# Performance work log

Measured on AMD Instinct MI355X. Metric: run time of the kernel, lower is better.

The kernel has to match this reference:

```python
import jax, jax.numpy as jnp
import numpy as np

B, N, C, L = 2, 128, 256, 3
NODE_IN, EDGE_IN = 128, 64
KN, KE = 101, 7
ALPHA = 0.2
EPS = 1e-5

def lrelu(x):
    return jax.nn.leaky_relu(x, ALPHA)

def layer_norm(x, g, b):
    mu = jnp.mean(x, axis=-1, keepdims=True)
    var = jnp.mean((x - mu) ** 2, axis=-1, keepdims=True)
    return (x - mu) / jnp.sqrt(var + EPS) * g + b

def setup_inputs() -> dict:
    key = jax.random.key(0)
    ks = jax.random.split(key, 20)
    s = 0.05
    nodes = jax.random.normal(ks[0], (B, N, NODE_IN), jnp.float32)
    edges = jax.random.normal(ks[1], (B, N, N, EDGE_IN), jnp.float32)
    m = (jax.random.uniform(ks[2], (B, N, N)) > 0.3).astype(jnp.float32)
    adj_mask = jnp.maximum(m, jnp.eye(N, dtype=jnp.float32)[None])  # guarantee non-empty rows
    return {
        'nodes': nodes, 'edges': edges, 'adj_mask': adj_mask,
        'pnW': jax.random.normal(ks[3], (C, NODE_IN)) * s, 'pnb': jnp.zeros((C,)),
        'peW': jax.random.normal(ks[4], (C, EDGE_IN)) * s, 'peb': jnp.zeros((C,)),
        'Wb': jax.random.normal(ks[5], (L, C, 3 * C)) * s,
        'Wbp': jax.random.normal(ks[6], (L, C, C)) * s,
        'Wfp': jax.random.normal(ks[7], (L, C, C)) * s,
        'ub': jax.random.normal(ks[8], (L, C)) * s,
        'Wf': jax.random.normal(ks[9], (L, C, C)) * s,
        'eln_g': jnp.ones((L, C)), 'eln_b': jnp.zeros((L, C)),
        'nln_g': jnp.ones((L, C)), 'nln_b': jnp.zeros((L, C)),
        'ncW': jax.random.normal(ks[10], (KN, C)) * s, 'ncb': jnp.zeros((KN,)),
        'ecW': jax.random.normal(ks[11], (KE, C)) * s, 'ecb': jnp.zeros((KE,)),
    }

def reference(nodes, edges, adj_mask, pnW, pnb, peW, peb, Wb, Wbp, Wfp, ub, Wf,
              eln_g, eln_b, nln_g, nln_b, ncW, ncb, ecW, ecb):
    nodes = nodes @ pnW.T + pnb          # (B,N,C)
    edges = edges @ peW.T + peb          # (B,N,N,C)
    mask3 = adj_mask[..., None]
    for l in range(Wb.shape[0]):
        Cd = nodes.shape[-1]
        Wb1, Wb2, Wb3 = Wb[l][:, :Cd], Wb[l][:, Cd:2 * Cd], Wb[l][:, 2 * Cd:]
        # W_b([f_i, edges, f_j]) without materializing the (B,N,N,3C) concat
        ai = nodes @ Wb1.T                # (B,N,C) broadcast along j
        aj = nodes @ Wb3.T                # (B,N,C) broadcast along i
        ne = lrelu(ai[:, :, None, :] + edges @ Wb2.T + aj[:, None, :, :])
        ne = ne * mask3
        new_edges = layer_norm(ne + edges, eln_g[l], eln_b[l])
        edges_in = jnp.swapaxes(new_edges, 1, 2)      # permute(0,2,1,3)
        tn = nodes @ Wfp[l].T             # shared by term_node_i / term_node_j
        st = edges_in @ Wbp[l].T + tn[:, :, None, :] + tn[:, None, :, :]
        r = lrelu(st @ ub[l])             # (B,N,N)
        r = jnp.where(adj_mask > 0, r, -jnp.inf)
        attn = jnp.nan_to_num(jax.nn.softmax(r, axis=2))
        agg = jnp.einsum('bij,bjd->bid', attn, nodes @ Wf[l].T)
        nodes = layer_norm(lrelu(agg) + nodes, nln_g[l], nln_b[l])
        edges = new_edges
    node_logits = nodes @ ncW.T + ncb
    edge_logits = edges @ ecW.T + ecb
    return (nodes, edges, node_logits, edge_logits)
```

## Files before the change

kernel.cpp:

```cpp
#include <hip/hip_runtime.h>
#include <hip/hip_bf16.h>


#define ALPHA 0.2f
#define EPS_ 1e-5f

typedef __hip_bfloat16 bf16;
typedef __bf16 bf16x8 __attribute__((ext_vector_type(8)));
typedef __bf16 bf16x4 __attribute__((ext_vector_type(4)));
typedef float floatx4 __attribute__((ext_vector_type(4)));

__device__ __forceinline__ float bf2f(bf16 x){ return __bfloat162float(x); }
__device__ __forceinline__ bf16  f2bf(float x){ return __float2bfloat16(x); }
__device__ __forceinline__ float lrelu_f(float x){ return x > 0.f ? x : ALPHA * x; }

#define T_NODES 0u
#define T_EDGES 32768u
#define T_ADJ   2129920u
#define T_PNW   2162688u
#define T_PNB   2195456u
#define T_PEW   2195712u
#define T_PEB   2212096u
#define T_WB    2212352u
#define T_WBP   2802176u
#define T_WFP   2998784u
#define T_UB    3195392u
#define T_WF    3196160u
#define T_ELNG  3392768u
#define T_ELNB  3393536u
#define T_NLNG  3394304u
#define T_NLNB  3395072u
#define T_NCW   3395840u
#define T_NCB   3421696u
#define T_ECW   3421800u
#define T_ECB   3423592u

#define O_NODES 0u
#define O_EDGES 65536u
#define O_NLOG  8454144u
#define O_ELOG  8480000u

struct SrcPtrs { const void* p[20]; };

__device__ __forceinline__ float rawld(const void* p, size_t i, bool isb){
    return isb ? bf2f(((const bf16*)p)[i]) : ((const float*)p)[i];
}

__device__ __forceinline__ bf16x8 ldfrag8(const void* p, size_t e, bool isb){
    if (isb) return *reinterpret_cast<const bf16x8*>((const bf16*)p + e);
    const float4* f = (const float4*)((const float*)p + e);
    float4 a = f[0], b = f[1];
    bf16 o[8];
    o[0]=f2bf(a.x); o[1]=f2bf(a.y); o[2]=f2bf(a.z); o[3]=f2bf(a.w);
    o[4]=f2bf(b.x); o[5]=f2bf(b.y); o[6]=f2bf(b.z); o[7]=f2bf(b.w);
    return *reinterpret_cast<bf16x8*>(o);
}

__global__ __launch_bounds__(256) void setup_k(SrcPtrs sp, bf16* __restrict__ canon,
                                               float* __restrict__ vbuf, float* __restrict__ wbuf,
                                               float* __restrict__ nodes_cur,
                                               bf16* __restrict__ rw2, bf16* __restrict__ rpe){
    const unsigned short* probe = (const unsigned short*)sp.p[12];
    const bool isb = (probe[0] == 0x3F80);
    int blk = blockIdx.x, tid = threadIdx.x;
    int wave = tid >> 6, lane = tid & 63, quad = lane >> 4, l16 = lane & 15;

    if (blk < 1024){
        const unsigned COFF[20] = {T_NODES,T_EDGES,T_ADJ,T_PNW,T_PNB,T_PEW,T_PEB,T_WB,T_WBP,T_WFP,
                                   T_UB,T_WF,T_ELNG,T_ELNB,T_NLNG,T_NLNB,T_NCW,T_NCB,T_ECW,T_ECB};
        const unsigned SZ[20]   = {32768u,2097152u,32768u,32768u,256u,16384u,256u,589824u,196608u,196608u,
                                   768u,196608u,768u,768u,768u,768u,25856u,101u,1792u,7u};
        unsigned gtid = blk*256u + tid;
        unsigned gstride = 1024u*256u;
        for (int t = 0; t < 20; ++t){
            const void* src = sp.p[t];
            unsigned coff = COFF[t], n = SZ[t];
            unsigned chunks = n >> 3;
            if (isb){
                const uint4* s4 = (const uint4*)src;
                for (unsigned idx = gtid; idx < chunks; idx += gstride)
                    *reinterpret_cast<uint4*>(canon + coff + idx*8u) = s4[idx];
            } else {
                const float4* s4 = (const float4*)src;
                for (unsigned idx = gtid; idx < chunks; idx += gstride){
                    float4 a = s4[2*idx], b = s4[2*idx+1];
                    bf16 o[8];
                    o[0]=f2bf(a.x); o[1]=f2bf(a.y); o[2]=f2bf(a.z); o[3]=f2bf(a.w);
                    o[4]=f2bf(b.x); o[5]=f2bf(b.y); o[6]=f2bf(b.z); o[7]=f2bf(b.w);
                    *reinterpret_cast<uint4*>(canon + coff + idx*8u) = *reinterpret_cast<uint4*>(o);
                }
            }
            unsigned tail = n & 7u;
            if (gtid < tail){
                unsigned li = chunks*8u + gtid;
                canon[coff + li] = isb ? ((const bf16*)src)[li] : f2bf(((const float*)src)[li]);
            }
        }
    } else if (blk < 1030){
        int q = blk - 1024;
        int l = q >> 1, m = q & 1;
        const void* W = m ? sp.p[9] : sp.p[8];
        float* out = (m ? wbuf : vbuf) + l*256;
        int c = tid;
        __shared__ float shu[256];
        shu[c] = rawld(sp.p[10], l*256 + c, isb);
        __syncthreads();
        float a0=0.f, a1=0.f, a2=0.f, a3=0.f;
        for (int cp0 = 0; cp0 < 256; cp0 += 16){
#pragma unroll
            for (int j = 0; j < 16; ++j){
                float wv = rawld(W, (size_t)l*65536u + (size_t)(cp0+j)*256u + c, isb);
                float pr = shu[cp0+j] * wv;
                if ((j & 3) == 0) a0 += pr;
                else if ((j & 3) == 1) a1 += pr;
                else if ((j & 3) == 2) a2 += pr;
                else a3 += pr;
            }
        }
        out[c] = (a0 + a1) + (a2 + a3);
    } else if (blk < 1038){
        int row0 = (blk - 1030) * 32;
        floatx4 acc[2][4] = {};
#pragma unroll
        for (int k0c = 0; k0c < 4; ++k0c){
            int k0 = k0c*32;
            bf16x8 a[2], bb[4];
#pragma unroll
            for (int mt = 0; mt < 2; ++mt)
                a[mt] = ldfrag8(sp.p[0], (size_t)(row0 + mt*16 + l16)*128u + k0 + quad*8, isb);
#pragma unroll
            for (int nt = 0; nt < 4; ++nt)
                bb[nt] = ldfrag8(sp.p[3], (size_t)(wave*64 + nt*16 + l16)*128u + k0 + quad*8, isb);
#pragma unroll
            for (int mt = 0; mt < 2; ++mt)
#pragma unroll
                for (int nt = 0; nt < 4; ++nt)
                    acc[mt][nt] = __builtin_amdgcn_mfma_f32_16x16x32_bf16(a[mt], bb[nt], acc[mt][nt], 0, 0, 0);
        }
#pragma unroll
        for (int nt = 0; nt < 4; ++nt){
            int n = wave*64 + nt*16 + l16;
            float bn = rawld(sp.p[4], n, isb);
#pragma unroll
            for (int mt = 0; mt < 2; ++mt)
#pragma unroll
                for (int reg = 0; reg < 4; ++reg){
                    int r = row0 + mt*16 + quad*4 + reg;
                    nodes_cur[r*256 + n] = acc[mt][nt][reg] + bn;
                }
        }
    } else if (blk < 1086){
        int rb = blk - 1038;
        int l = rb >> 4, n_tile = rb & 15;
        bf16* dst = rw2 + l*65536;
#pragma unroll
        for (int half = 0; half < 2; ++half){
            int slot = half*256 + tid;
            int k0c = slot >> 6, ln = slot & 63;
            int qd = ln >> 4, lw = ln & 15;
            int n = n_tile*16 + lw;
            bf16 o[8];
#pragma unroll
            for (int j = 0; j < 8; ++j){
                int k = k0c*32 + qd*8 + j;
                o[j] = f2bf(rawld(sp.p[7], (size_t)l*196608u + (size_t)n*768u + 256u + k, isb));
            }
            *reinterpret_cast<uint4*>(dst + ((k0c*16 + n_tile)*64 + ln)*8) = *reinterpret_cast<uint4*>(o);
        }
    } else {
        int n_tile = blk - 1086;
        if (tid < 128){
            int slot = tid;
            int k0c = slot >> 6, ln = slot & 63;
            int qd = ln >> 4, lw = ln & 15;
            int n = n_tile*16 + lw;
            bf16 o[8];
#pragma unroll
            for (int j = 0; j < 8; ++j){
                int k = k0c*32 + qd*8 + j;
                o[j] = f2bf(rawld(sp.p[5], (size_t)n*64u + k, isb));
            }
            *reinterpret_cast<uint4*>(rpe + ((n_tile*2 + k0c)*64 + ln)*8) = *reinterpret_cast<uint4*>(o);
        }
    }
}

__global__ __launch_bounds__(256) void node_linears_k(
        const float* __restrict__ nodes_cur, const bf16* __restrict__ Wb_l,
        const bf16* __restrict__ Wf_l, const float* __restrict__ w_l,
        float* __restrict__ ai, float* __restrict__ aj,
        float* __restrict__ nf, float* __restrict__ s){
    int row = blockIdx.x;
    int c = threadIdx.x;
    __shared__ float x[256];
    __shared__ float red[4];
    x[c] = nodes_cur[row*256 + c];
    __syncthreads();
    float xs = x[c] * w_l[c];
    for (int off = 32; off; off >>= 1) xs += __shfl_xor(xs, off, 64);
    if ((c & 63) == 0) red[c >> 6] = xs;
    const bf16x8* w1 = reinterpret_cast<const bf16x8*>(Wb_l + (size_t)c*768);
    const bf16x8* w3 = reinterpret_cast<const bf16x8*>(Wb_l + (size_t)c*768 + 512);
    const bf16x8* wf = reinterpret_cast<const bf16x8*>(Wf_l + (size_t)c*256);
    float a1 = 0.f, a3 = 0.f, f = 0.f;
#pragma unroll 4
    for (int ch = 0; ch < 32; ++ch){
        bf16x8 v1 = w1[ch], v3 = w3[ch], vf = wf[ch];
#pragma unroll
        for (int j = 0; j < 8; ++j){
            float xv = x[ch*8 + j];
            a1 += xv * (float)v1[j];
            a3 += xv * (float)v3[j];
            f  += xv * (float)vf[j];
        }
    }
    ai[row*256 + c] = a1;
    aj[row*256 + c] = a3;
    nf[row*256 + c] = f;
    __syncthreads();
    if (c == 0) s[row] = red[0] + red[1] + red[2] + red[3];
}

__global__ __launch_bounds__(256) void edge_update2_k(
        bf16* __restrict__ Ebuf, const bf16* __restrict__ rw2_l,
        const float* __restrict__ ai, const float* __restrict__ aj,
        const bf16* __restrict__ adj, const bf16* __restrict__ g, const bf16* __restrict__ bta,
        const float* __restrict__ v, float* __restrict__ rbuf,
        int isfinal, const bf16* __restrict__ ecW, const bf16* __restrict__ ecb,
        void* __restrict__ dout, const unsigned short* __restrict__ probe,
        int isfirst, const bf16* __restrict__ eIn, const bf16* __restrict__ rpe,
        const bf16* __restrict__ peb){
    int row0 = blockIdx.x * 64;
    int b = row0 >> 14, i = (row0 >> 7) & 127, j0 = row0 & 127;
    int tid = threadIdx.x;
    int wave = tid >> 6, lane = tid & 63, quad = lane >> 4, l16 = lane & 15;

    __shared__ bf16  shA[64*264];
    __shared__ float sh_ai[256];
    __shared__ float sh_v[256];
    __shared__ float sh_g[256];
    __shared__ float sh_bt[256];
    __shared__ float sh_w7[7][256];
    __shared__ float smS[4][64];
    __shared__ float smQ[4][64];
    __shared__ float dvp[4][64];
    __shared__ float lgp[4][64][7];

    sh_ai[tid] = ai[(b*128 + i)*256 + tid];
    sh_v[tid]  = v[tid];
    sh_g[tid]  = bf2f(g[tid]);
    sh_bt[tid] = bf2f(bta[tid]);
    if (isfirst){
        floatx4 pacc[4][4] = {};
#pragma unroll
        for (int k0c = 0; k0c < 2; ++k0c){
            int k0 = k0c*32;
            bf16x8 a[4], bb[4];
#pragma unroll
            for (int mt = 0; mt < 4; ++mt)
                a[mt] = *reinterpret_cast<const bf16x8*>(eIn + (size_t)(row0 + mt*16 + l16)*64 + k0 + quad*8);
#pragma unroll
            for (int nt = 0; nt < 4; ++nt)
                bb[nt] = *reinterpret_cast<const bf16x8*>(rpe + ((size_t)((wave*4 + nt)*2 + k0c)*64 + lane)*8);
#pragma unroll
            for (int mt = 0; mt < 4; ++mt)
#pragma unroll
                for (int nt = 0; nt < 4; ++nt)
                    pacc[mt][nt] = __builtin_amdgcn_mfma_f32_16x16x32_bf16(a[mt], bb[nt], pacc[mt][nt], 0, 0, 0);
        }
#pragma unroll
        for (int nt = 0; nt < 4; ++nt){
            int col = wave*64 + nt*16 + l16;
            float bbv = bf2f(peb[col]);
#pragma unroll
            for (int mt = 0; mt < 4; ++mt)
#pragma unroll
                for (int reg = 0; reg < 4; ++reg)
                    shA[(mt*16 + quad*4 + reg)*264 + col] = f2bf(pacc[mt][nt][reg] + bbv);
        }
    } else {
#pragma unroll
        for (int it = 0; it < 8; ++it){
            int idx = it*256 + tid;
            int r = idx >> 5, c8 = idx & 31;
            bf16x8 vA = *reinterpret_cast<const bf16x8*>(Ebuf + (size_t)(row0 + r)*256 + c8*8);
            *reinterpret_cast<bf16x8*>(&shA[r*264 + c8*8]) = vA;
        }
    }
    if (isfinal){
        for (int idx = tid; idx < 7*256; idx += 256)
            sh_w7[idx >> 8][idx & 255] = bf2f(ecW[idx]);
    }
    __syncthreads();

    floatx4 acc[4][4] = {};
    {
        const bf16* shb = &shA[l16*264];
        for (int k0c = 0; k0c < 8; ++k0c){
            bf16x8 bfr[4];
#pragma unroll
            for (int rf = 0; rf < 4; ++rf)
                bfr[rf] = *reinterpret_cast<const bf16x8*>(shb + rf*16*264 + k0c*32 + quad*8);
#pragma unroll
            for (int mt = 0; mt < 4; ++mt){
                bf16x8 afrag = *reinterpret_cast<const bf16x8*>(
                    rw2_l + ((size_t)(k0c*16 + wave*4 + mt)*64 + lane)*8);
#pragma unroll
                for (int rf = 0; rf < 4; ++rf)
                    acc[mt][rf] = __builtin_amdgcn_mfma_f32_16x16x32_bf16(afrag, bfr[rf], acc[mt][rf], 0, 0, 0);
            }
        }
    }

    const bool isb = (probe[0] == 0x3F80);
    float maskv[4];
#pragma unroll
    for (int rf = 0; rf < 4; ++rf){
        int rl = rf*16 + l16;
        int j  = j0 + rl;
        maskv[rf] = bf2f(adj[(b*128 + i)*128 + j]);
        const float* ajrow = aj + (size_t)(b*128 + j)*256;
        float s = 0.f, q = 0.f;
#pragma unroll
        for (int mt = 0; mt < 4; ++mt){
            int c0 = wave*64 + mt*16 + quad*4;
            float4 ajv = *reinterpret_cast<const float4*>(ajrow + c0);
            float4 aiv = *reinterpret_cast<const float4*>(sh_ai + c0);
            bf16x4 ev  = *reinterpret_cast<const bf16x4*>(&shA[rl*264 + c0]);
#pragma unroll
            for (int reg = 0; reg < 4; ++reg){
                float y = acc[mt][rf][reg] + ((const float*)&aiv)[reg] + ((const float*)&ajv)[reg];
                float x = lrelu_f(y) * maskv[rf] + (float)ev[reg];
                acc[mt][rf][reg] = x;
                s += x; q += x*x;
            }
        }
        s += __shfl_xor(s, 16, 64); s += __shfl_xor(s, 32, 64);
        q += __shfl_xor(q, 16, 64); q += __shfl_xor(q, 32, 64);
        if (quad == 0){ smS[wave][rl] = s; smQ[wave][rl] = q; }
    }
    __syncthreads();

#pragma unroll
    for (int rf = 0; rf < 4; ++rf){
        int rl = rf*16 + l16;
        int j  = j0 + rl;
        int grow = row0 + rl;
        float ts = smS[0][rl] + smS[1][rl] + smS[2][rl] + smS[3][rl];
        float tq = smQ[0][rl] + smQ[1][rl] + smQ[2][rl] + smQ[3][rl];
        float mu  = ts * (1.f/256.f);
        float var = tq * (1.f/256.f) - mu*mu;
        float rstd = rsqrtf(var + EPS_);
        float dv = 0.f;
        float lg[7] = {0.f,0.f,0.f,0.f,0.f,0.f,0.f};
#pragma unroll
        for (int mt = 0; mt < 4; ++mt){
            int c0 = wave*64 + mt*16 + quad*4;
            float4 gv = *reinterpret_cast<const float4*>(sh_g + c0);
            float4 bv = *reinterpret_cast<const float4*>(sh_bt + c0);
            float4 vv = *reinterpret_cast<const float4*>(sh_v + c0);
            float xo4[4];
#pragma unroll
            for (int reg = 0; reg < 4; ++reg){
                float xo = (acc[mt][rf][reg] - mu) * rstd * ((const float*)&gv)[reg] + ((const float*)&bv)[reg];
                xo4[reg] = xo;
                dv += xo * ((const float*)&vv)[reg];
            }
            if (!isfinal){
                bf16x4 ob;
#pragma unroll
                for (int reg = 0; reg < 4; ++reg) ob[reg] = f2bf(xo4[reg]);
                *reinterpret_cast<bf16x4*>(Ebuf + (size_t)grow*256 + c0) = ob;
            } else {
                if (isb){
                    bf16x4 ob;
#pragma unroll
                    for (int reg = 0; reg < 4; ++reg) ob[reg] = f2bf(xo4[reg]);
                    *reinterpret_cast<bf16x4*>((bf16*)dout + O_EDGES + (size_t)grow*256 + c0) = ob;
                } else {
                    float4 of;
                    of.x = xo4[0]; of.y = xo4[1]; of.z = xo4[2]; of.w = xo4[3];
                    *reinterpret_cast<float4*>((float*)dout + O_EDGES + (size_t)grow*256 + c0) = of;
                }
#pragma unroll
                for (int k = 0; k < 7; ++k){
                    const float* w7r = &sh_w7[k][c0];
#pragma unroll
                    for (int reg = 0; reg < 4; ++reg) lg[k] += xo4[reg] * w7r[reg];
                }
            }
        }
        dv += __shfl_xor(dv, 16, 64); dv += __shfl_xor(dv, 32, 64);
        if (quad == 0) dvp[wave][rl] = dv;
        if (isfinal){
#pragma unroll
            for (int k = 0; k < 7; ++k){
                lg[k] += __shfl_xor(lg[k], 16, 64);
                lg[k] += __shfl_xor(lg[k], 32, 64);
            }
            if (quad == 0){
#pragma unroll
                for (int k = 0; k < 7; ++k) lgp[wave][rl][k] = lg[k];
            }
        }
    }
    __syncthreads();

    if (wave == 0 && quad == 0){
#pragma unroll
        for (int rf = 0; rf < 4; ++rf){
            int rl = rf*16 + l16;
            int j  = j0 + rl;
            int grow = row0 + rl;
            float d = dvp[0][rl] + dvp[1][rl] + dvp[2][rl] + dvp[3][rl];
            rbuf[(b*128 + j)*128 + i] = d;
            if (isfinal){
#pragma unroll
                for (int k = 0; k < 7; ++k){
                    float val = lgp[0][rl][k] + lgp[1][rl][k] + lgp[2][rl][k] + lgp[3][rl][k] + bf2f(ecb[k]);
                    if (isb) ((bf16*)dout)[O_ELOG + (size_t)grow*7 + k] = f2bf(val);
                    else     ((float*)dout)[O_ELOG + (size_t)grow*7 + k] = val;
                }
            }
        }
    }
}

__global__ __launch_bounds__(256) void node_update_k(
        const float* __restrict__ rbuf, const float* __restrict__ s_in, const bf16* __restrict__ adj,
        const float* __restrict__ nf_in, float* __restrict__ nodes_cur,
        const bf16* __restrict__ g, const bf16* __restrict__ bta,
        int isfinal,
        const bf16* __restrict__ Wb_nx, const bf16* __restrict__ Wf_nx, const float* __restrict__ w_nx,
        float* __restrict__ ai_o, float* __restrict__ aj_o, float* __restrict__ nf_o, float* __restrict__ s_o,
        const bf16* __restrict__ ncW, const bf16* __restrict__ ncb,
        void* __restrict__ dout, const unsigned short* __restrict__ probe){
    int row = blockIdx.x;
    int b = row >> 7;
    int tid = threadIdx.x;
    int wave = tid >> 6, lane = tid & 63;
    __shared__ float attn[128];
    __shared__ float shr[16];
    __shared__ float shfx[256];

    float rv = -__builtin_inff();
    if (tid < 128){
        float t = rbuf[row*128 + tid] + s_in[row] + s_in[b*128 + tid];
        t = lrelu_f(t);
        rv = (bf2f(adj[row*128 + tid]) > 0.f) ? t : -__builtin_inff();
    }
    float m = rv;
    for (int off = 32; off; off >>= 1) m = fmaxf(m, __shfl_xor(m, off, 64));
    if (lane == 0) shr[wave] = m;
    __syncthreads();
    float mx = fmaxf(fmaxf(shr[0], shr[1]), fmaxf(shr[2], shr[3]));
    float e = (tid < 128 && rv > -__builtin_inff()) ? expf(rv - mx) : 0.f;
    if (tid < 128) attn[tid] = e;
    float se = e;
    for (int off = 32; off; off >>= 1) se += __shfl_xor(se, off, 64);
    if (lane == 0) shr[4 + wave] = se;
    __syncthreads();
    float inv = 1.f / (shr[4] + shr[5] + shr[6] + shr[7]);

    int c = tid;
    const float* nfb = nf_in + (size_t)b*32768 + c;
    float g0 = 0.f, g1 = 0.f, g2 = 0.f, g3 = 0.f;
    float g4 = 0.f, g5 = 0.f, g6 = 0.f, g7 = 0.f;
    for (int jj = 0; jj < 128; jj += 8){
        g0 += attn[jj]   * nfb[(size_t)jj*256];
        g1 += attn[jj+1] * nfb[(size_t)(jj+1)*256];
        g2 += attn[jj+2] * nfb[(size_t)(jj+2)*256];
        g3 += attn[jj+3] * nfb[(size_t)(jj+3)*256];
        g4 += attn[jj+4] * nfb[(size_t)(jj+4)*256];
        g5 += attn[jj+5] * nfb[(size_t)(jj+5)*256];
        g6 += attn[jj+6] * nfb[(size_t)(jj+6)*256];
        g7 += attn[jj+7] * nfb[(size_t)(jj+7)*256];
    }
    float agg = (((g0 + g1) + (g2 + g3)) + ((g4 + g5) + (g6 + g7))) * inv;
    float x = lrelu_f(agg) + nodes_cur[row*256 + c];
    float xs = x, xq = x*x;
    for (int off = 32; off; off >>= 1){ xs += __shfl_xor(xs, off, 64); xq += __shfl_xor(xq, off, 64); }
    if (lane == 0){ shr[8 + wave] = xs; shr[12 + wave] = xq; }
    __syncthreads();
    float sum = shr[8] + shr[9] + shr[10] + shr[11];
    float sq  = shr[12] + shr[13] + shr[14] + shr[15];
    float mu  = sum * (1.f/256.f);
    float var = sq * (1.f/256.f) - mu*mu;
    float rstd = rsqrtf(var + EPS_);
    float out = (x - mu) * rstd * bf2f(g[c]) + bf2f(bta[c]);
    nodes_cur[row*256 + c] = out;
    shfx[c] = out;
    __syncthreads();

    if (!isfinal){
        float ws2 = out * w_nx[c];
        for (int off = 32; off; off >>= 1) ws2 += __shfl_xor(ws2, off, 64);
        if (lane == 0) shr[wave] = ws2;
        const bf16x8* w1 = reinterpret_cast<const bf16x8*>(Wb_nx + (size_t)c*768);
        const bf16x8* w3 = reinterpret_cast<const bf16x8*>(Wb_nx + (size_t)c*768 + 512);
        const bf16x8* wf = reinterpret_cast<const bf16x8*>(Wf_nx + (size_t)c*256);
        float a1 = 0.f, a3 = 0.f, f = 0.f;
#pragma unroll 4
        for (int ch = 0; ch < 32; ++ch){
            bf16x8 v1 = w1[ch], v3 = w3[ch], vf = wf[ch];
#pragma unroll
            for (int j = 0; j < 8; ++j){
                float xv = shfx[ch*8 + j];
                a1 += xv * (float)v1[j];
                a3 += xv * (float)v3[j];
                f  += xv * (float)vf[j];
            }
        }
        ai_o[row*256 + c] = a1;
        aj_o[row*256 + c] = a3;
        nf_o[row*256 + c] = f;
        __syncthreads();
        if (c == 0) s_o[row] = shr[0] + shr[1] + shr[2] + shr[3];
    } else {
        const bool isb = (probe[0] == 0x3F80);
        if (isb) ((bf16*)dout)[O_NODES + row*256 + c] = f2bf(out);
        else     ((float*)dout)[O_NODES + row*256 + c] = out;
        if (tid < 101){
            const bf16x8* wr = reinterpret_cast<const bf16x8*>(ncW + (size_t)tid*256);
            float acc = bf2f(ncb[tid]);
#pragma unroll 4
            for (int ch = 0; ch < 32; ++ch){
                bf16x8 wv = wr[ch];
#pragma unroll
                for (int j = 0; j < 8; ++j) acc += shfx[ch*8 + j] * (float)wv[j];
            }
            if (isb) ((bf16*)dout)[O_NLOG + row*101 + tid] = f2bf(acc);
            else     ((float*)dout)[O_NLOG + row*101 + tid] = acc;
        }
    }
}

extern "C" void kernel_launch(void* const* d_in, const int* in_sizes, int n_in,
                              void* d_out, int out_size, void* d_ws, size_t ws_size,
                              hipStream_t stream){
    (void)in_sizes; (void)n_in; (void)out_size; (void)ws_size;

    SrcPtrs sp;
    for (int i = 0; i < 20; ++i) sp.p[i] = d_in[i];
    const unsigned short* probe = (const unsigned short*)d_in[12];

    bf16* canon = (bf16*)d_ws;
    char* ws2 = (char*)d_ws + 6847488;
    bf16* Ebuf = (bf16*)ws2;
    float* f = (float*)(ws2 + 16777216);
    float* ai    = f;
    float* aj    = f + 65536;
    float* nfA   = f + 131072;
    float* nfB   = f + 196608;
    float* sA    = f + 262144;
    float* sB    = f + 262400;
    float* rbuf  = f + 262656;
    float* vbuf  = f + 295424;
    float* wbuf  = f + 296192;
    float* nodes_cur = f + 296960;
    bf16* rw2 = (bf16*)(f + 362496);
    bf16* rpe = rw2 + 196608;

    const bf16* c_edges = canon + T_EDGES;
    const bf16* c_adj   = canon + T_ADJ;
    const bf16* c_peb   = canon + T_PEB;
    const bf16* c_Wb    = canon + T_WB;
    const bf16* c_Wf    = canon + T_WF;
    const bf16* c_elng  = canon + T_ELNG;
    const bf16* c_elnb  = canon + T_ELNB;
    const bf16* c_nlng  = canon + T_NLNG;
    const bf16* c_nlnb  = canon + T_NLNB;
    const bf16* c_ncW   = canon + T_NCW;
    const bf16* c_ncb   = canon + T_NCB;
    const bf16* c_ecW   = canon + T_ECW;
    const bf16* c_ecb   = canon + T_ECB;

    setup_k<<<dim3(1102), dim3(256), 0, stream>>>(sp, canon, vbuf, wbuf, nodes_cur, rw2, rpe);
    node_linears_k<<<dim3(256), dim3(256), 0, stream>>>(
        nodes_cur, c_Wb, c_Wf, wbuf, ai, aj, nfA, sA);

    for (int l = 0; l < 3; ++l){
        int fin = (l == 2);
        int fst = (l == 0);
        float* nf_in = (l & 1) ? nfB : nfA;
        float* nf_out = (l & 1) ? nfA : nfB;
        float* s_in  = (l & 1) ? sB : sA;
        float* s_out = (l & 1) ? sA : sB;
        edge_update2_k<<<dim3(512), dim3(256), 0, stream>>>(
            Ebuf, rw2 + l*65536, ai, aj, c_adj,
            c_elng + l*256, c_elnb + l*256, vbuf + l*256, rbuf,
            fin, c_ecW, c_ecb, d_out, probe,
            fst, c_edges, rpe, c_peb);
        node_update_k <<<dim3(256), dim3(256), 0, stream>>>(
            rbuf, s_in, c_adj, nf_in, nodes_cur, c_nlng + l*256, c_nlnb + l*256,
            fin,
            c_Wb + (size_t)(l+1)*196608, c_Wf + (size_t)(l+1)*65536, wbuf + (l+1)*256,
            ai, aj, nf_out, s_out,
            c_ncW, c_ncb, d_out, probe);
    }
}
```

Measured before the change: 274.5 us.

## Move node linears to MFMA kernel and halve edge tile rows

The per-row scalar node linear projections (ai, aj, nf) are replaced by a separate MFMA-based kernel that processes 32 rows per block, and they are no longer fused into node_update_k. The edge update kernel now handles 32 rows per block instead of 64, with twice the blocks and a launch-bounds occupancy hint, and it prefetches the aj values and mask early. This trades extra kernel launches and lower per-block reuse of the rw2 weights for tensor-core node GEMMs and more parallelism and occupancy in the edge kernel. The linears kernel runs only 8 blocks, which may underuse the GPU, and node inputs are now rounded to bf16 before the product.

Measured after the change: 327.0 us. 19.1% more time.

```diff
diff --git a/kernel.cpp b/kernel.cpp
--- a/kernel.cpp
+++ b/kernel.cpp
@@ -185,43 +185,76 @@
     }
 }
 
-__global__ __launch_bounds__(256) void node_linears_k(
-        const float* __restrict__ nodes_cur, const bf16* __restrict__ Wb_l,
-        const bf16* __restrict__ Wf_l, const float* __restrict__ w_l,
+__global__ __launch_bounds__(256) void linears_k(
+        const float* __restrict__ nodes_cur,
+        const bf16* __restrict__ Wb_l, const bf16* __restrict__ Wf_l,
+        const float* __restrict__ w_l,
         float* __restrict__ ai, float* __restrict__ aj,
         float* __restrict__ nf, float* __restrict__ s){
-    int row = blockIdx.x;
-    int c = threadIdx.x;
-    __shared__ float x[256];
-    __shared__ float red[4];
-    x[c] = nodes_cur[row*256 + c];
+    int row0 = blockIdx.x * 32;
+    int tid = threadIdx.x;
+    int wave = tid >> 6, lane = tid & 63, quad = lane >> 4, l16 = lane & 15;
+    __shared__ bf16 shX[32*264];
+
+#pragma unroll
+    for (int it = 0; it < 4; ++it){
+        int idx = it*256 + tid;
+        int r = idx >> 5, c8 = idx & 31;
+        const float4* fp = (const float4*)(nodes_cur + (size_t)(row0 + r)*256 + c8*8);
+        float4 a = fp[0], b2 = fp[1];
+        bf16 o[8];
+        o[0]=f2bf(a.x); o[1]=f2bf(a.y); o[2]=f2bf(a.z); o[3]=f2bf(a.w);
+        o[4]=f2bf(b2.x); o[5]=f2bf(b2.y); o[6]=f2bf(b2.z); o[7]=f2bf(b2.w);
+        *reinterpret_cast<uint4*>(&shX[r*264 + c8*8]) = *reinterpret_cast<uint4*>(o);
+    }
     __syncthreads();
-    float xs = x[c] * w_l[c];
-    for (int off = 32; off; off >>= 1) xs += __shfl_xor(xs, off, 64);
-    if ((c & 63) == 0) red[c >> 6] = xs;
-    const bf16x8* w1 = reinterpret_cast<const bf16x8*>(Wb_l + (size_t)c*768);
-    const bf16x8* w3 = reinterpret_cast<const bf16x8*>(Wb_l + (size_t)c*768 + 512);
-    const bf16x8* wf = reinterpret_cast<const bf16x8*>(Wf_l + (size_t)c*256);
-    float a1 = 0.f, a3 = 0.f, f = 0.f;
-#pragma unroll 4
-    for (int ch = 0; ch < 32; ++ch){
-        bf16x8 v1 = w1[ch], v3 = w3[ch], vf = wf[ch];
-#pragma unroll
-        for (int j = 0; j < 8; ++j){
-            float xv = x[ch*8 + j];
-            a1 += xv * (float)v1[j];
-            a3 += xv * (float)v3[j];
-            f  += xv * (float)vf[j];
-        }
-    }
-    ai[row*256 + c] = a1;
-    aj[row*256 + c] = a3;
-    nf[row*256 + c] = f;
-    __syncthreads();
-    if (c == 0) s[row] = red[0] + red[1] + red[2] + red[3];
+
+    floatx4 acc[2][12] = {};
+    for (int k0c = 0; k0c < 8; ++k0c){
+        int k0 = k0c*32 + quad*8;
+        bf16x8 a[2];
+#pragma unroll
+        for (int mt = 0; mt < 2; ++mt)
+            a[mt] = *reinterpret_cast<const bf16x8*>(&shX[(mt*16 + l16)*264 + k0]);
+#pragma unroll
+        for (int nt = 0; nt < 12; ++nt){
+            int t = wave*12 + nt;
+            int n = (t & 15)*16 + l16;
+            const bf16* bp;
+            if (t < 16)      bp = Wb_l + (size_t)n*768 + k0;
+            else if (t < 32) bp = Wb_l + (size_t)n*768 + 512 + k0;
+            else             bp = Wf_l + (size_t)n*256 + k0;
+            bf16x8 bb = *reinterpret_cast<const bf16x8*>(bp);
+#pragma unroll
+            for (int mt = 0; mt < 2; ++mt)
+                acc[mt][nt] = __builtin_amdgcn_mfma_f32_16x16x32_bf16(a[mt], bb, acc[mt][nt], 0, 0, 0);
+        }
+    }
+#pragma unroll
+    for (int nt = 0; nt < 12; ++nt){
+        int t = wave*12 + nt;
+        int n = (t & 15)*16 + l16;
+        float* out = (t < 16) ? ai : (t < 32) ? aj : nf;
+#pragma unroll
+        for (int mt = 0; mt < 2; ++mt)
+#pragma unroll
+            for (int reg = 0; reg < 4; ++reg)
+                out[(size_t)(row0 + mt*16 + quad*4 + reg)*256 + n] = acc[mt][nt][reg];
+    }
+    if (tid < 32){
+        const bf16* xr = &shX[tid*264];
+        float a0=0.f, a1=0.f, a2=0.f, a3=0.f;
+        for (int c = 0; c < 256; c += 4){
+            a0 += (float)xr[c]   * w_l[c];
+            a1 += (float)xr[c+1] * w_l[c+1];
+            a2 += (float)xr[c+2] * w_l[c+2];
+            a3 += (float)xr[c+3] * w_l[c+3];
+        }
+        s[row0 + tid] = (a0 + a1) + (a2 + a3);
+    }
 }
 
-__global__ __launch_bounds__(256) void edge_update2_k(
+__global__ __launch_bounds__(256, 3) void edge_update2_k(
         bf16* __restrict__ Ebuf, const bf16* __restrict__ rw2_l,
         const float* __restrict__ ai, const float* __restrict__ aj,
         const bf16* __restrict__ adj, const bf16* __restrict__ g, const bf16* __restrict__ bta,
@@ -230,40 +263,52 @@
         void* __restrict__ dout, const unsigned short* __restrict__ probe,
         int isfirst, const bf16* __restrict__ eIn, const bf16* __restrict__ rpe,
         const bf16* __restrict__ peb){
-    int row0 = blockIdx.x * 64;
+    int row0 = blockIdx.x * 32;
     int b = row0 >> 14, i = (row0 >> 7) & 127, j0 = row0 & 127;
     int tid = threadIdx.x;
     int wave = tid >> 6, lane = tid & 63, quad = lane >> 4, l16 = lane & 15;
 
-    __shared__ bf16  shA[64*264];
+    __shared__ bf16  shA[32*264];
     __shared__ float sh_ai[256];
     __shared__ float sh_v[256];
     __shared__ float sh_g[256];
     __shared__ float sh_bt[256];
     __shared__ float sh_w7[7][256];
-    __shared__ float smS[4][64];
-    __shared__ float smQ[4][64];
-    __shared__ float dvp[4][64];
-    __shared__ float lgp[4][64][7];
+    __shared__ float smS[4][32];
+    __shared__ float smQ[4][32];
+    __shared__ float dvp[4][32];
+    __shared__ float lgp[4][32][7];
+
+    float maskv[2];
+    float4 ajp[2][4];
+#pragma unroll
+    for (int rf = 0; rf < 2; ++rf){
+        int j = j0 + rf*16 + l16;
+        maskv[rf] = bf2f(adj[(b*128 + i)*128 + j]);
+        const float* ajrow = aj + (size_t)(b*128 + j)*256 + wave*64;
+#pragma unroll
+        for (int mt = 0; mt < 4; ++mt)
+            ajp[rf][mt] = *reinterpret_cast<const float4*>(ajrow + mt*16 + quad*4);
+    }
 
     sh_ai[tid] = ai[(b*128 + i)*256 + tid];
     sh_v[tid]  = v[tid];
     sh_g[tid]  = bf2f(g[tid]);
     sh_bt[tid] = bf2f(bta[tid]);
     if (isfirst){
-        floatx4 pacc[4][4] = {};
+        floatx4 pacc[2][4] = {};
 #pragma unroll
         for (int k0c = 0; k0c < 2; ++k0c){
             int k0 = k0c*32;
-            bf16x8 a[4], bb[4];
-#pragma unroll
-            for (int mt = 0; mt < 4; ++mt)
+            bf16x8 a[2], bb[4];
+#pragma unroll
+            for (int mt = 0; mt < 2; ++mt)
                 a[mt] = *reinterpret_cast<const bf16x8*>(eIn + (size_t)(row0 + mt*16 + l16)*64 + k0 + quad*8);
 #pragma unroll
             for (int nt = 0; nt < 4; ++nt)
                 bb[nt] = *reinterpret_cast<const bf16x8*>(rpe + ((size_t)((wave*4 + nt)*2 + k0c)*64 + lane)*8);
 #pragma unroll
-            for (int mt = 0; mt < 4; ++mt)
+            for (int mt = 0; mt < 2; ++mt)
 #pragma unroll
                 for (int nt = 0; nt < 4; ++nt)
                     pacc[mt][nt] = __builtin_amdgcn_mfma_f32_16x16x32_bf16(a[mt], bb[nt], pacc[mt][nt], 0, 0, 0);
@@ -273,14 +318,14 @@
             int col = wave*64 + nt*16 + l16;
             float bbv = bf2f(peb[col]);
 #pragma unroll
-            for (int mt = 0; mt < 4; ++mt)
+            for (int mt = 0; mt < 2; ++mt)
 #pragma unroll
                 for (int reg = 0; reg < 4; ++reg)
                     shA[(mt*16 + quad*4 + reg)*264 + col] = f2bf(pacc[mt][nt][reg] + bbv);
         }
     } else {
 #pragma unroll
-        for (int it = 0; it < 8; ++it){
+        for (int it = 0; it < 4; ++it){
             int idx = it*256 + tid;
             int r = idx >> 5, c8 = idx & 31;
             bf16x8 vA = *reinterpret_cast<const bf16x8*>(Ebuf + (size_t)(row0 + r)*256 + c8*8);
@@ -293,58 +338,52 @@
     }
     __syncthreads();
 
-    floatx4 acc[4][4] = {};
+    floatx4 acc[4][2] = {};
     {
         const bf16* shb = &shA[l16*264];
         for (int k0c = 0; k0c < 8; ++k0c){
-            bf16x8 bfr[4];
-#pragma unroll
-            for (int rf = 0; rf < 4; ++rf)
+            bf16x8 bfr[2];
+#pragma unroll
+            for (int rf = 0; rf < 2; ++rf)
                 bfr[rf] = *reinterpret_cast<const bf16x8*>(shb + rf*16*264 + k0c*32 + quad*8);
 #pragma unroll
             for (int mt = 0; mt < 4; ++mt){
                 bf16x8 afrag = *reinterpret_cast<const bf16x8*>(
                     rw2_l + ((size_t)(k0c*16 + wave*4 + mt)*64 + lane)*8);
 #pragma unroll
-                for (int rf = 0; rf < 4; ++rf)
+                for (int rf = 0; rf < 2; ++rf)
                     acc[mt][rf] = __builtin_amdgcn_mfma_f32_16x16x32_bf16(afrag, bfr[rf], acc[mt][rf], 0, 0, 0);
             }
         }
     }
 
     const bool isb = (probe[0] == 0x3F80);
-    float maskv[4];
-#pragma unroll
-    for (int rf = 0; rf < 4; ++rf){
+#pragma unroll
+    for (int rf = 0; rf < 2; ++rf){
         int rl = rf*16 + l16;
-        int j  = j0 + rl;
-        maskv[rf] = bf2f(adj[(b*128 + i)*128 + j]);
-        const float* ajrow = aj + (size_t)(b*128 + j)*256;
-        float s = 0.f, q = 0.f;
+        float sm = 0.f, q = 0.f;
 #pragma unroll
         for (int mt = 0; mt < 4; ++mt){
             int c0 = wave*64 + mt*16 + quad*4;
-            float4 ajv = *reinterpret_cast<const float4*>(ajrow + c0);
             float4 aiv = *reinterpret_cast<const float4*>(sh_ai + c0);
             bf16x4 ev  = *reinterpret_cast<const bf16x4*>(&shA[rl*264 + c0]);
 #pragma unroll
             for (int reg = 0; reg < 4; ++reg){
-                float y = acc[mt][rf][reg] + ((const float*)&aiv)[reg] + ((const float*)&ajv)[reg];
+                float y = acc[mt][rf][reg] + ((const float*)&aiv)[reg] + ((const float*)&ajp[rf][mt])[reg];
                 float x = lrelu_f(y) * maskv[rf] + (float)ev[reg];
                 acc[mt][rf][reg] = x;
-                s += x; q += x*x;
-            }
-        }
-        s += __shfl_xor(s, 16, 64); s += __shfl_xor(s, 32, 64);
-        q += __shfl_xor(q, 16, 64); q += __shfl_xor(q, 32, 64);
-        if (quad == 0){ smS[wave][rl] = s; smQ[wave][rl] = q; }
+                sm += x; q += x*x;
+            }
+        }
+        sm += __shfl_xor(sm, 16, 64); sm += __shfl_xor(sm, 32, 64);
+        q  += __shfl_xor(q, 16, 64);  q  += __shfl_xor(q, 32, 64);
+        if (quad == 0){ smS[wave][rl] = sm; smQ[wave][rl] = q; }
     }
     __syncthreads();
 
 #pragma unroll
-    for (int rf = 0; rf < 4; ++rf){
+    for (int rf = 0; rf < 2; ++rf){
         int rl = rf*16 + l16;
-        int j  = j0 + rl;
         int grow = row0 + rl;
         float ts = smS[0][rl] + smS[1][rl] + smS[2][rl] + smS[3][rl];
         float tq = smQ[0][rl] + smQ[1][rl] + smQ[2][rl] + smQ[3][rl];
@@ -408,7 +447,7 @@
 
     if (wave == 0 && quad == 0){
 #pragma unroll
-        for (int rf = 0; rf < 4; ++rf){
+        for (int rf = 0; rf < 2; ++rf){
             int rl = rf*16 + l16;
             int j  = j0 + rl;
             int grow = row0 + rl;
@@ -431,8 +470,6 @@
         const float* __restrict__ nf_in, float* __restrict__ nodes_cur,
         const bf16* __restrict__ g, const bf16* __restrict__ bta,
         int isfinal,
-        const bf16* __restrict__ Wb_nx, const bf16* __restrict__ Wf_nx, const float* __restrict__ w_nx,
-        float* __restrict__ ai_o, float* __restrict__ aj_o, float* __restrict__ nf_o, float* __restrict__ s_o,
         const bf16* __restrict__ ncW, const bf16* __restrict__ ncb,
         void* __restrict__ dout, const unsigned short* __restrict__ probe){
     int row = blockIdx.x;
@@ -489,35 +526,11 @@
     float rstd = rsqrtf(var + EPS_);
     float out = (x - mu) * rstd * bf2f(g[c]) + bf2f(bta[c]);
     nodes_cur[row*256 + c] = out;
-    shfx[c] = out;
-    __syncthreads();
-
-    if (!isfinal){
-        float ws2 = out * w_nx[c];
-        for (int off = 32; off; off >>= 1) ws2 += __shfl_xor(ws2, off, 64);
-        if (lane == 0) shr[wave] = ws2;
-        const bf16x8* w1 = reinterpret_cast<const bf16x8*>(Wb_nx + (size_t)c*768);
-        const bf16x8* w3 = reinterpret_cast<const bf16x8*>(Wb_nx + (size_t)c*768 + 512);
-        const bf16x8* wf = reinterpret_cast<const bf16x8*>(Wf_nx + (size_t)c*256);
-        float a1 = 0.f, a3 = 0.f, f = 0.f;
-#pragma unroll 4
-        for (int ch = 0; ch < 32; ++ch){
-            bf16x8 v1 = w1[ch], v3 = w3[ch], vf = wf[ch];
-#pragma unroll
-            for (int j = 0; j < 8; ++j){
-                float xv = shfx[ch*8 + j];
-                a1 += xv * (float)v1[j];
-                a3 += xv * (float)v3[j];
-                f  += xv * (float)vf[j];
-            }
-        }
-        ai_o[row*256 + c] = a1;
-        aj_o[row*256 + c] = a3;
-        nf_o[row*256 + c] = f;
+
+    if (isfinal){
+        const bool isb = (probe[0] == 0x3F80);
+        shfx[c] = out;
         __syncthreads();
-        if (c == 0) s_o[row] = shr[0] + shr[1] + shr[2] + shr[3];
-    } else {
-        const bool isb = (probe[0] == 0x3F80);
         if (isb) ((bf16*)dout)[O_NODES + row*256 + c] = f2bf(out);
         else     ((float*)dout)[O_NODES + row*256 + c] = out;
         if (tid < 101){
@@ -576,7 +589,7 @@
     const bf16* c_ecb   = canon + T_ECB;
 
     setup_k<<<dim3(1102), dim3(256), 0, stream>>>(sp, canon, vbuf, wbuf, nodes_cur, rw2, rpe);
-    node_linears_k<<<dim3(256), dim3(256), 0, stream>>>(
+    linears_k<<<dim3(8), dim3(256), 0, stream>>>(
         nodes_cur, c_Wb, c_Wf, wbuf, ai, aj, nfA, sA);
 
     for (int l = 0; l < 3; ++l){
@@ -586,16 +599,18 @@
         float* nf_out = (l & 1) ? nfA : nfB;
         float* s_in  = (l & 1) ? sB : sA;
         float* s_out = (l & 1) ? sA : sB;
-        edge_update2_k<<<dim3(512), dim3(256), 0, stream>>>(
+        edge_update2_k<<<dim3(1024), dim3(256), 0, stream>>>(
             Ebuf, rw2 + l*65536, ai, aj, c_adj,
             c_elng + l*256, c_elnb + l*256, vbuf + l*256, rbuf,
             fin, c_ecW, c_ecb, d_out, probe,
             fst, c_edges, rpe, c_peb);
         node_update_k <<<dim3(256), dim3(256), 0, stream>>>(
             rbuf, s_in, c_adj, nf_in, nodes_cur, c_nlng + l*256, c_nlnb + l*256,
-            fin,
-            c_Wb + (size_t)(l+1)*196608, c_Wf + (size_t)(l+1)*65536, wbuf + (l+1)*256,
-            ai, aj, nf_out, s_out,
-            c_ncW, c_ncb, d_out, probe);
+            fin, c_ncW, c_ncb, d_out, probe);
+        if (!fin){
+            linears_k<<<dim3(8), dim3(256), 0, stream>>>(
+                nodes_cur, c_Wb + (size_t)(l+1)*196608, c_Wf + (size_t)(l+1)*65536,
+                wbuf + (l+1)*256, ai, aj, nf_out, s_out);
+        }
     }
 }
```

## Halve edge-update tile to 32 rows, stage output in LDS for coalesced stores

Applied to the files above, without the earlier changes.

Shrinks the edge-update kernel's row tile from 64 to 32 rows and doubles the grid to 1024 blocks. It also adds a launch-bounds occupancy hint so more blocks fit per CU. The aj and adjacency-mask loads are hoisted to the kernel start to overlap with the GEMM. Normalized edges are written back into shared memory and then stored to global with coalesced 16-byte writes, instead of scattered 8-byte stores from the MFMA layout. The trade-off is less reuse of each weight fragment loaded from global, since every block reloads the full rw2 weights for fewer rows, plus an extra LDS round trip.

Result: faster. 263.6 us (-4.0%).

```diff
diff --git a/kernel.cpp b/kernel.cpp
--- a/kernel.cpp
+++ b/kernel.cpp
@@ -221,7 +221,7 @@
     if (c == 0) s[row] = red[0] + red[1] + red[2] + red[3];
 }
 
-__global__ __launch_bounds__(256) void edge_update2_k(
+__global__ __launch_bounds__(256, 3) void edge_update2_k(
         bf16* __restrict__ Ebuf, const bf16* __restrict__ rw2_l,
         const float* __restrict__ ai, const float* __restrict__ aj,
         const bf16* __restrict__ adj, const bf16* __restrict__ g, const bf16* __restrict__ bta,
@@ -230,40 +230,52 @@
         void* __restrict__ dout, const unsigned short* __restrict__ probe,
         int isfirst, const bf16* __restrict__ eIn, const bf16* __restrict__ rpe,
         const bf16* __restrict__ peb){
-    int row0 = blockIdx.x * 64;
+    int row0 = blockIdx.x * 32;
     int b = row0 >> 14, i = (row0 >> 7) & 127, j0 = row0 & 127;
     int tid = threadIdx.x;
     int wave = tid >> 6, lane = tid & 63, quad = lane >> 4, l16 = lane & 15;
 
-    __shared__ bf16  shA[64*264];
+    __shared__ bf16  shA[32*264];
     __shared__ float sh_ai[256];
     __shared__ float sh_v[256];
     __shared__ float sh_g[256];
     __shared__ float sh_bt[256];
     __shared__ float sh_w7[7][256];
-    __shared__ float smS[4][64];
-    __shared__ float smQ[4][64];
-    __shared__ float dvp[4][64];
-    __shared__ float lgp[4][64][7];
+    __shared__ float smS[4][32];
+    __shared__ float smQ[4][32];
+    __shared__ float dvp[4][32];
+    __shared__ float lgp[4][32][7];
+
+    float maskv[2];
+    float4 ajp[2][4];
+#pragma unroll
+    for (int rf = 0; rf < 2; ++rf){
+        int j = j0 + rf*16 + l16;
+        maskv[rf] = bf2f(adj[(b*128 + i)*128 + j]);
+        const float* ajrow = aj + (size_t)(b*128 + j)*256 + wave*64;
+#pragma unroll
+        for (int mt = 0; mt < 4; ++mt)
+            ajp[rf][mt] = *reinterpret_cast<const float4*>(ajrow + mt*16 + quad*4);
+    }
 
     sh_ai[tid] = ai[(b*128 + i)*256 + tid];
     sh_v[tid]  = v[tid];
     sh_g[tid]  = bf2f(g[tid]);
     sh_bt[tid] = bf2f(bta[tid]);
     if (isfirst){
-        floatx4 pacc[4][4] = {};
+        floatx4 pacc[2][4] = {};
 #pragma unroll
         for (int k0c = 0; k0c < 2; ++k0c){
             int k0 = k0c*32;
-            bf16x8 a[4], bb[4];
-#pragma unroll
-            for (int mt = 0; mt < 4; ++mt)
+            bf16x8 a[2], bb[4];
+#pragma unroll
+            for (int mt = 0; mt < 2; ++mt)
                 a[mt] = *reinterpret_cast<const bf16x8*>(eIn + (size_t)(row0 + mt*16 + l16)*64 + k0 + quad*8);
 #pragma unroll
             for (int nt = 0; nt < 4; ++nt)
                 bb[nt] = *reinterpret_cast<const bf16x8*>(rpe + ((size_t)((wave*4 + nt)*2 + k0c)*64 + lane)*8);
 #pragma unroll
-            for (int mt = 0; mt < 4; ++mt)
+            for (int mt = 0; mt < 2; ++mt)
 #pragma unroll
                 for (int nt = 0; nt < 4; ++nt)
                     pacc[mt][nt] = __builtin_amdgcn_mfma_f32_16x16x32_bf16(a[mt], bb[nt], pacc[mt][nt], 0, 0, 0);
@@ -273,14 +285,14 @@
             int col = wave*64 + nt*16 + l16;
             float bbv = bf2f(peb[col]);
 #pragma unroll
-            for (int mt = 0; mt < 4; ++mt)
+            for (int mt = 0; mt < 2; ++mt)
 #pragma unroll
                 for (int reg = 0; reg < 4; ++reg)
                     shA[(mt*16 + quad*4 + reg)*264 + col] = f2bf(pacc[mt][nt][reg] + bbv);
         }
     } else {
 #pragma unroll
-        for (int it = 0; it < 8; ++it){
+        for (int it = 0; it < 4; ++it){
             int idx = it*256 + tid;
             int r = idx >> 5, c8 = idx & 31;
             bf16x8 vA = *reinterpret_cast<const bf16x8*>(Ebuf + (size_t)(row0 + r)*256 + c8*8);
@@ -293,59 +305,52 @@
     }
     __syncthreads();
 
-    floatx4 acc[4][4] = {};
+    floatx4 acc[4][2] = {};
     {
         const bf16* shb = &shA[l16*264];
         for (int k0c = 0; k0c < 8; ++k0c){
-            bf16x8 bfr[4];
-#pragma unroll
-            for (int rf = 0; rf < 4; ++rf)
+            bf16x8 bfr[2];
+#pragma unroll
+            for (int rf = 0; rf < 2; ++rf)
                 bfr[rf] = *reinterpret_cast<const bf16x8*>(shb + rf*16*264 + k0c*32 + quad*8);
 #pragma unroll
             for (int mt = 0; mt < 4; ++mt){
                 bf16x8 afrag = *reinterpret_cast<const bf16x8*>(
                     rw2_l + ((size_t)(k0c*16 + wave*4 + mt)*64 + lane)*8);
 #pragma unroll
-                for (int rf = 0; rf < 4; ++rf)
+                for (int rf = 0; rf < 2; ++rf)
                     acc[mt][rf] = __builtin_amdgcn_mfma_f32_16x16x32_bf16(afrag, bfr[rf], acc[mt][rf], 0, 0, 0);
             }
         }
     }
 
     const bool isb = (probe[0] == 0x3F80);
-    float maskv[4];
-#pragma unroll
-    for (int rf = 0; rf < 4; ++rf){
+#pragma unroll
+    for (int rf = 0; rf < 2; ++rf){
         int rl = rf*16 + l16;
-        int j  = j0 + rl;
-        maskv[rf] = bf2f(adj[(b*128 + i)*128 + j]);
-        const float* ajrow = aj + (size_t)(b*128 + j)*256;
-        float s = 0.f, q = 0.f;
+        float sm = 0.f, q = 0.f;
 #pragma unroll
         for (int mt = 0; mt < 4; ++mt){
             int c0 = wave*64 + mt*16 + quad*4;
-            float4 ajv = *reinterpret_cast<const float4*>(ajrow + c0);
             float4 aiv = *reinterpret_cast<const float4*>(sh_ai + c0);
             bf16x4 ev  = *reinterpret_cast<const bf16x4*>(&shA[rl*264 + c0]);
 #pragma unroll
             for (int reg = 0; reg < 4; ++reg){
-                float y = acc[mt][rf][reg] + ((const float*)&aiv)[reg] + ((const float*)&ajv)[reg];
+                float y = acc[mt][rf][reg] + ((const float*)&aiv)[reg] + ((const float*)&ajp[rf][mt])[reg];
                 float x = lrelu_f(y) * maskv[rf] + (float)ev[reg];
                 acc[mt][rf][reg] = x;
-                s += x; q += x*x;
-            }
-        }
-        s += __shfl_xor(s, 16, 64); s += __shfl_xor(s, 32, 64);
-        q += __shfl_xor(q, 16, 64); q += __shfl_xor(q, 32, 64);
-        if (quad == 0){ smS[wave][rl] = s; smQ[wave][rl] = q; }
-    }
-    __syncthreads();
-
-#pragma unroll
-    for (int rf = 0; rf < 4; ++rf){
+                sm += x; q += x*x;
+            }
+        }
+        sm += __shfl_xor(sm, 16, 64); sm += __shfl_xor(sm, 32, 64);
+        q  += __shfl_xor(q, 16, 64);  q  += __shfl_xor(q, 32, 64);
+        if (quad == 0){ smS[wave][rl] = sm; smQ[wave][rl] = q; }
+    }
+    __syncthreads();
+
+#pragma unroll
+    for (int rf = 0; rf < 2; ++rf){
         int rl = rf*16 + l16;
-        int j  = j0 + rl;
-        int grow = row0 + rl;
         float ts = smS[0][rl] + smS[1][rl] + smS[2][rl] + smS[3][rl];
         float tq = smQ[0][rl] + smQ[1][rl] + smQ[2][rl] + smQ[3][rl];
         float mu  = ts * (1.f/256.f);
@@ -359,36 +364,18 @@
             float4 gv = *reinterpret_cast<const float4*>(sh_g + c0);
             float4 bv = *reinterpret_cast<const float4*>(sh_bt + c0);
             float4 vv = *reinterpret_cast<const float4*>(sh_v + c0);
-            float xo4[4];
+            bf16x4 ob;
 #pragma unroll
             for (int reg = 0; reg < 4; ++reg){
                 float xo = (acc[mt][rf][reg] - mu) * rstd * ((const float*)&gv)[reg] + ((const float*)&bv)[reg];
-                xo4[reg] = xo;
+                ob[reg] = f2bf(xo);
                 dv += xo * ((const float*)&vv)[reg];
-            }
-            if (!isfinal){
-                bf16x4 ob;
-#pragma unroll
-                for (int reg = 0; reg < 4; ++reg) ob[reg] = f2bf(xo4[reg]);
-                *reinterpret_cast<bf16x4*>(Ebuf + (size_t)grow*256 + c0) = ob;
-            } else {
-                if (isb){
-                    bf16x4 ob;
-#pragma unroll
-                    for (int reg = 0; reg < 4; ++reg) ob[reg] = f2bf(xo4[reg]);
-                    *reinterpret_cast<bf16x4*>((bf16*)dout + O_EDGES + (size_t)grow*256 + c0) = ob;
-                } else {
-                    float4 of;
-                    of.x = xo4[0]; of.y = xo4[1]; of.z = xo4[2]; of.w = xo4[3];
-                    *reinterpret_cast<float4*>((float*)dout + O_EDGES + (size_t)grow*256 + c0) = of;
+                if (isfinal){
+#pragma unroll
+                    for (int k = 0; k < 7; ++k) lg[k] += xo * sh_w7[k][c0 + reg];
                 }
-#pragma unroll
-                for (int k = 0; k < 7; ++k){
-                    const float* w7r = &sh_w7[k][c0];
-#pragma unroll
-                    for (int reg = 0; reg < 4; ++reg) lg[k] += xo4[reg] * w7r[reg];
-                }
-            }
+            }
+            *reinterpret_cast<bf16x4*>(&shA[rl*264 + c0]) = ob;
         }
         dv += __shfl_xor(dv, 16, 64); dv += __shfl_xor(dv, 32, 64);
         if (quad == 0) dvp[wave][rl] = dv;
@@ -406,9 +393,40 @@
     }
     __syncthreads();
 
+    if (!isfinal){
+#pragma unroll
+        for (int it = 0; it < 4; ++it){
+            int idx = it*256 + tid;
+            int r = idx >> 5, c8 = idx & 31;
+            *reinterpret_cast<bf16x8*>(Ebuf + (size_t)(row0 + r)*256 + c8*8) =
+                *reinterpret_cast<const bf16x8*>(&shA[r*264 + c8*8]);
+        }
+    } else if (isb){
+#pragma unroll
+        for (int it = 0; it < 4; ++it){
+            int idx = it*256 + tid;
+            int r = idx >> 5, c8 = idx & 31;
+            *reinterpret_cast<bf16x8*>((bf16*)dout + O_EDGES + (size_t)(row0 + r)*256 + c8*8) =
+                *reinterpret_cast<const bf16x8*>(&shA[r*264 + c8*8]);
+        }
+    } else {
+#pragma unroll
+        for (int it = 0; it < 4; ++it){
+            int idx = it*256 + tid;
+            int r = idx >> 5, c8 = idx & 31;
+            bf16x8 vA = *reinterpret_cast<const bf16x8*>(&shA[r*264 + c8*8]);
+            float4 f0, f1;
+            f0.x = (float)vA[0]; f0.y = (float)vA[1]; f0.z = (float)vA[2]; f0.w = (float)vA[3];
+            f1.x = (float)vA[4]; f1.y = (float)vA[5]; f1.z = (float)vA[6]; f1.w = (float)vA[7];
+            float* op = (float*)dout + O_EDGES + (size_t)(row0 + r)*256 + c8*8;
+            *reinterpret_cast<float4*>(op)     = f0;
+            *reinterpret_cast<float4*>(op + 4) = f1;
+        }
+    }
+
     if (wave == 0 && quad == 0){
 #pragma unroll
-        for (int rf = 0; rf < 4; ++rf){
+        for (int rf = 0; rf < 2; ++rf){
             int rl = rf*16 + l16;
             int j  = j0 + rl;
             int grow = row0 + rl;
@@ -586,7 +604,7 @@
         float* nf_out = (l & 1) ? nfA : nfB;
         float* s_in  = (l & 1) ? sB : sA;
         float* s_out = (l & 1) ? sA : sB;
-        edge_update2_k<<<dim3(512), dim3(256), 0, stream>>>(
+        edge_update2_k<<<dim3(1024), dim3(256), 0, stream>>>(
             Ebuf, rw2 + l*65536, ai, aj, c_adj,
             c_elng + l*256, c_elnb + l*256, vbuf + l*256, rbuf,
             fin, c_ecW, c_ecb, d_out, probe,
```
